# Optimization experiments

Measured on AMD Instinct MI355X. Metric: run time of the kernel, lower is better.

The kernel has to match this reference:

```python
import jax, jax.numpy as jnp
import numpy as np

B, C, HW, A, E, H1, HID = 4096, 4, 64, 32, 4, 1024, 512


def setup_inputs() -> dict:
    key = jax.random.key(0)
    ks = jax.random.split(key, 16)
    def rn(k, shape, fan_in):
        return jax.random.normal(k, shape, dtype=jnp.float32) / np.sqrt(fan_in)
    inp = {
        "x": jax.random.normal(ks[0], (B, C, HW, HW), dtype=jnp.float32),
        # conv stack (OIHW)
        "cW1": rn(ks[1], (32, C, 8, 8), C * 64), "cb1": 0.1 * jnp.ones((32,), jnp.float32),
        "cW2": rn(ks[2], (64, 32, 4, 4), 32 * 16), "cb2": 0.1 * jnp.ones((64,), jnp.float32),
        "cW3": rn(ks[3], (64, 64, 3, 3), 64 * 9), "cb3": 0.1 * jnp.ones((64,), jnp.float32),
        # E expert advantage streams: Linear(1024->512), relu, Linear(512->A)
        "aW1": rn(ks[4], (E, H1, HID), H1), "ab1": jnp.zeros((E, HID), jnp.float32),
        "aW2": rn(ks[5], (E, HID, A), HID), "ab2": jnp.zeros((E, A), jnp.float32),
        # E expert value streams: Linear(1024->512), relu, Linear(512->1)
        "vW1": rn(ks[6], (E, H1, HID), H1), "vb1": jnp.zeros((E, HID), jnp.float32),
        "vW2": rn(ks[7], (E, HID, 1), HID), "vb2": jnp.zeros((E, 1), jnp.float32),
        # reward bucket boundaries (buffer): boundaries * scale - 1e-8
        "boundaries": jnp.array([-0.5, 0.0, 0.5], jnp.float32) * 1.0 - 1e-8,
    }
    return inp


def _conv(h, W, b, stride):
    out = jax.lax.conv_general_dilated(h, W, (stride, stride), "VALID",
                                       dimension_numbers=("NCHW", "OIHW", "NCHW"))
    return out + b[None, :, None, None]


def _routed_mlp(h, W1, b1, W2, b2, idx):
    # h: [B, H1]; W1: [E, H1, HID]; W2: [E, HID, O]; idx: [B]
    # Compute all experts (E is tiny), then gather the routed output per sample.
    z = jax.nn.relu(jnp.einsum("bi,eio->ebo", h, W1) + b1[:, None, :])  # [E,B,HID]
    y = jnp.einsum("ebo,eoa->eba", z, W2) + b2[:, None, :]              # [E,B,O]
    return y[idx, jnp.arange(h.shape[0])]                                # [B,O]


def reference(x, cW1, cb1, cW2, cb2, cW3, cb3, aW1, ab1, aW2, ab2,
              vW1, vb1, vW2, vb2, boundaries):
    h = jax.nn.relu(_conv(x, cW1, cb1, 4))   # [B,32,15,15]
    h = jax.nn.relu(_conv(h, cW2, cb2, 2))   # [B,64,6,6]
    h = jax.nn.relu(_conv(h, cW3, cb3, 1))   # [B,64,4,4]
    bsz = x.shape[0]
    h = h.reshape(bsz, -1)                   # [B,1024]
    rewards = x[:, -1, 0, 0]                 # [B]
    idx = jnp.sum(rewards[:, None] > boundaries[None, :], axis=1)  # [B] in [0,E)
    ya = _routed_mlp(h, aW1, ab1, aW2, ab2, idx)  # [B,A]
    mean = jnp.sum(ya, axis=1, keepdims=True) / ya.shape[1]
    ys = _routed_mlp(h, vW1, vb1, vW2, vb2, idx)  # [B,1]
    q = (ya - mean) + ys
    return q
```

## Files before the change

### kernel.cpp

```cpp
#include <hip/hip_runtime.h>
#include <hip/hip_bf16.h>

typedef __bf16 bf16;
typedef bf16 bf16x8 __attribute__((ext_vector_type(8)));
typedef bf16 bf16x4 __attribute__((ext_vector_type(4)));
typedef float f32x4 __attribute__((ext_vector_type(4)));

__device__ __forceinline__ int SZ(int a) { return a ^ (((a >> 7) & 7) << 4); }

__global__ __launch_bounds__(256) void k_pre(const float* __restrict__ cW1,
    const float* __restrict__ cW2, const float* __restrict__ cW3,
    bf16* __restrict__ W1p, bf16* __restrict__ W2p, bf16* __restrict__ W3p) {
  const int bid = blockIdx.x, tid = threadIdx.x;
  if (bid < 32) {
    int i = bid * 256 + tid;
    int oc = i >> 8, k = i & 255;
    int ic = k & 3, kp = k >> 2, kx = kp & 7, ky = kp >> 3;
    W1p[i] = (bf16)cW1[oc * 256 + ic * 64 + ky * 8 + kx];
  } else if (bid < 160) {
    int i = (bid - 32) * 256 + tid;
    int oc = i >> 9, k = i & 511;
    int ic = k & 31, kp = k >> 5, kx = kp & 3, ky = kp >> 2;
    W2p[i] = (bf16)cW2[oc * 512 + ic * 16 + ky * 4 + kx];
  } else {
    int i = (bid - 160) * 256 + tid;
    if (i < 36864) {
      int oc = i / 576, k = i - oc * 576;
      int ic = k & 63, kp = k >> 6, kx = kp % 3, ky = kp / 3;
      W3p[i] = (bf16)cW3[oc * 576 + ic * 9 + ky * 3 + kx];
    }
  }
}

__global__ __launch_bounds__(256) void k_pre2(const float* __restrict__ aW1,
    const float* __restrict__ vW1, bf16* __restrict__ W1T) {
  __shared__ float t[64][65];
  const int bid2 = blockIdx.x;
  const int bz = bid2 >> 7, rest = bid2 & 127, by = rest >> 4, bx = rest & 15;
  const float* in = (bz >= 4 ? vW1 : aW1) + (size_t)(bz & 3) * 524288;
  const int k0 = bx * 64, n0 = by * 64;
  const int tid = threadIdx.x, cc = tid & 63, r0 = (tid >> 6) * 16;
  for (int i = 0; i < 16; ++i)
    t[r0 + i][cc] = in[(size_t)(k0 + r0 + i) * 512 + n0 + cc];
  __syncthreads();
  for (int i = 0; i < 16; ++i) {
    int n = r0 + i, k = cc;
    W1T[((size_t)bz * 512 + n0 + n) * 1024 + k0 + k] = (bf16)t[k][n];
  }
}

__global__ __launch_bounds__(1024) void k_route(const float* __restrict__ x,
    const float* __restrict__ bd, int* __restrict__ perm, int* __restrict__ cnt) {
  const int tid = threadIdx.x;
  const float t0 = bd[0], t1 = bd[1], t2 = bd[2];
  int e[4];
  #pragma unroll
  for (int i = 0; i < 4; ++i) {
    const int b = tid * 4 + i;
    const float r = x[(size_t)b * 16384 + 12288];
    e[i] = (r > t0) + (r > t1) + (r > t2);
  }
  int lc[4] = {0, 0, 0, 0};
  #pragma unroll
  for (int i = 0; i < 4; ++i) lc[e[i]]++;
  const int lane = tid & 63, wv = tid >> 6;
  __shared__ int wsum[16][4];
  __shared__ int wbase[16][4];
  int pre[4];
  #pragma unroll
  for (int q = 0; q < 4; ++q) {
    int v = lc[q];
    #pragma unroll
    for (int d = 1; d < 64; d <<= 1) {
      int u = __shfl_up(v, d);
      if (lane >= d) v += u;
    }
    pre[q] = v - lc[q];
    if (lane == 63) wsum[wv][q] = v;
  }
  __syncthreads();
  if (tid == 0) {
    int tot[4] = {0, 0, 0, 0};
    for (int w = 0; w < 16; ++w)
      #pragma unroll
      for (int q = 0; q < 4; ++q) { wbase[w][q] = tot[q]; tot[q] += wsum[w][q]; }
    #pragma unroll
    for (int q = 0; q < 4; ++q) cnt[q] = tot[q];
  }
  __syncthreads();
  int run[4];
  #pragma unroll
  for (int q = 0; q < 4; ++q) run[q] = wbase[wv][q] + pre[q];
  #pragma unroll
  for (int i = 0; i < 4; ++i) {
    const int b = tid * 4 + i;
    perm[e[i] * 4096 + run[e[i]]] = b;
    run[e[i]]++;
  }
}

__global__ __launch_bounds__(256, 4) void k_conv1(const float* __restrict__ x,
    const bf16* __restrict__ W1p, const float* __restrict__ b1,
    bf16* __restrict__ h1) {
  __shared__ bf16 sA[16384];
  const int b = blockIdx.x, tid = threadIdx.x;
  const int lane = tid & 63, wave = tid >> 6, lid = lane & 15, c = lane >> 4;
  const int ot = wave & 1, col = ot * 16 + lid;

  bf16x8 bw[8];
  #pragma unroll
  for (int ks = 0; ks < 8; ++ks) bw[ks] = *(const bf16x8*)(W1p + col * 256 + ks * 32 + c * 8);
  const float bias = b1[col];
  #pragma unroll
  for (int ks = 0; ks < 8; ++ks) asm volatile("" : "+v"(bw[ks]));

  {
    const float4* xs = (const float4*)(x + (size_t)b * 16384);
    #pragma unroll
    for (int hb = 0; hb < 2; ++hb) {
      float4 r[2][4];
      #pragma unroll
      for (int h = 0; h < 2; ++h)
        #pragma unroll
        for (int ic = 0; ic < 4; ++ic)
          r[h][ic] = xs[ic * 1024 + tid + (hb * 2 + h) * 256];
      #pragma unroll
      for (int h = 0; h < 2; ++h) {
        const int g = tid + (hb * 2 + h) * 256;
        bf16x8 lo, hi;
        lo[0] = (bf16)r[h][0].x; lo[1] = (bf16)r[h][1].x; lo[2] = (bf16)r[h][2].x; lo[3] = (bf16)r[h][3].x;
        lo[4] = (bf16)r[h][0].y; lo[5] = (bf16)r[h][1].y; lo[6] = (bf16)r[h][2].y; lo[7] = (bf16)r[h][3].y;
        hi[0] = (bf16)r[h][0].z; hi[1] = (bf16)r[h][1].z; hi[2] = (bf16)r[h][2].z; hi[3] = (bf16)r[h][3].z;
        hi[4] = (bf16)r[h][0].w; hi[5] = (bf16)r[h][1].w; hi[6] = (bf16)r[h][2].w; hi[7] = (bf16)r[h][3].w;
        *(bf16x8*)((char*)sA + SZ(g * 32))      = lo;
        *(bf16x8*)((char*)sA + SZ(g * 32 + 16)) = hi;
      }
    }
  }
  __syncthreads();

  int ab[8], ptv[8];
  #pragma unroll
  for (int pi = 0; pi < 8; ++pi) {
    int pt = (wave >> 1) + 2 * pi; if (pt > 14) pt = 14;
    ptv[pi] = pt;
    int p = pt * 16 + lid; if (p > 224) p = 224;
    const int py = p / 15, px = p - py * 15;
    ab[pi] = py * 2048 + px * 32 + c * 16;
  }
  f32x4 acc[8];
  #pragma unroll
  for (int pi = 0; pi < 8; ++pi) acc[pi] = (f32x4){0.f, 0.f, 0.f, 0.f};
  #pragma unroll
  for (int ks = 0; ks < 8; ++ks)
    #pragma unroll
    for (int pi = 0; pi < 8; ++pi)
      acc[pi] = __builtin_amdgcn_mfma_f32_16x16x32_bf16(
          *(const bf16x8*)((const char*)sA + SZ(ab[pi] + ks * 512)), bw[ks], acc[pi], 0, 0, 0);
  __syncthreads();

  #pragma unroll
  for (int pi = 0; pi < 8; ++pi)
    #pragma unroll
    for (int r = 0; r < 4; ++r) {
      const int pr = ptv[pi] * 16 + c * 4 + r;
      if (pr < 225) sA[pr * 32 + col] = (bf16)fmaxf(acc[pi][r] + bias, 0.f);
    }
  __syncthreads();

  bf16* hb = h1 + (size_t)b * 7200;
  for (int i = tid; i < 900; i += 256)
    *(bf16x8*)(hb + i * 8) = *(const bf16x8*)(&sA[i * 8]);
}

__global__ __launch_bounds__(256, 3) void k_conv23(const bf16* __restrict__ h1,
    const bf16* __restrict__ W2p, const float* __restrict__ b2,
    const bf16* __restrict__ W3p, const float* __restrict__ b3,
    bf16* __restrict__ h3) {
  __shared__ bf16 sh1[2][9000];
  __shared__ bf16 sh2[2][2592];
  const int b0 = blockIdx.x * 2, tid = threadIdx.x;
  const int lane = tid & 63, wave = tid >> 6, lid = lane & 15, c = lane >> 4;
  const int col = wave * 16 + lid;

  bf16x8 bw2[16];
  #pragma unroll
  for (int ks = 0; ks < 16; ++ks) bw2[ks] = *(const bf16x8*)(W2p + col * 512 + ks * 32 + c * 8);
  const float bias2 = b2[col];
  #pragma unroll
  for (int ks = 0; ks < 16; ++ks) asm volatile("" : "+v"(bw2[ks]));

  for (int i = tid; i < 1800; i += 256) {
    const int img = (i >= 900), j = i - img * 900;
    const int pix = j >> 2, part = j & 3;
    *(bf16x8*)(&sh1[img][pix * 40 + part * 8]) =
        *(const bf16x8*)(h1 + (size_t)(b0 + img) * 7200 + j * 8);
  }
  __syncthreads();

  f32x4 acc2[2][3];
  #pragma unroll
  for (int g = 0; g < 2; ++g)
    #pragma unroll
    for (int pt = 0; pt < 3; ++pt) acc2[g][pt] = (f32x4){0.f, 0.f, 0.f, 0.f};
  #pragma unroll
  for (int g = 0; g < 2; ++g) {
    int abase[3];
    #pragma unroll
    for (int pt = 0; pt < 3; ++pt) {
      int p = pt * 16 + lid; if (p > 35) p = 35;
      const int oy = p / 6, ox = p - oy * 6;
      abase[pt] = (oy * 30 + ox * 2) * 40 + c * 8;
    }
    #pragma unroll
    for (int ks = 0; ks < 16; ++ks) {
      const int ky = ks >> 2, kx = ks & 3;
      #pragma unroll
      for (int pt = 0; pt < 3; ++pt)
        acc2[g][pt] = __builtin_amdgcn_mfma_f32_16x16x32_bf16(
            *(const bf16x8*)(&sh1[g][abase[pt] + (ky * 15 + kx) * 40]), bw2[ks],
            acc2[g][pt], 0, 0, 0);
    }
  }
  #pragma unroll
  for (int g = 0; g < 2; ++g)
    #pragma unroll
    for (int pt = 0; pt < 3; ++pt)
      #pragma unroll
      for (int r = 0; r < 4; ++r) {
        const int pr = pt * 16 + c * 4 + r;
        if (pr < 36) sh2[g][pr * 72 + col] = (bf16)fmaxf(acc2[g][pt][r] + bias2, 0.f);
      }
  __syncthreads();

  bf16x8 bw3[18];
  #pragma unroll
  for (int ks = 0; ks < 18; ++ks) bw3[ks] = *(const bf16x8*)(W3p + col * 576 + ks * 32 + c * 8);
  const float bias3 = b3[col];
  const int oy = lid >> 2, ox = lid & 3;
  const int ab3 = (oy * 6 + ox) * 72 + c * 8;
  #pragma unroll
  for (int g = 0; g < 2; ++g) {
    f32x4 acc = {0.f, 0.f, 0.f, 0.f};
    #pragma unroll
    for (int ks = 0; ks < 18; ++ks) {
      const int kp = ks >> 1, ky = kp / 3, kx = kp - ky * 3;
      acc = __builtin_amdgcn_mfma_f32_16x16x32_bf16(
          *(const bf16x8*)(&sh2[g][ab3 + (ky * 6 + kx) * 72 + (ks & 1) * 32]), bw3[ks],
          acc, 0, 0, 0);
    }
    bf16x4 o;
    #pragma unroll
    for (int r = 0; r < 4; ++r) o[r] = (bf16)fmaxf(acc[r] + bias3, 0.f);
    *(bf16x4*)(h3 + (size_t)(b0 + g) * 1024 + col * 16 + c * 4) = o;
  }
}

__global__ __launch_bounds__(512) void k_mlp1(const bf16* __restrict__ h3,
    const bf16* __restrict__ W1T, const float* __restrict__ ab1, const float* __restrict__ vb1,
    const int* __restrict__ perm, const int* __restrict__ cnt,
    bf16* __restrict__ za, bf16* __restrict__ zv) {
  const int e = blockIdx.z;
  const int cntE = cnt[e];
  const int m0 = blockIdx.x * 64;
  if (m0 >= cntE) return;
  const int n0 = blockIdx.y * 128;
  const bf16* WA = W1T + (size_t)e * 524288;
  const bf16* WV = W1T + (size_t)(4 + e) * 524288;

  __shared__ bf16 As[64 * 72];
  __shared__ int rows[64];
  const int tid = threadIdx.x;
  if (tid < 64) {
    int j = m0 + tid; if (j > cntE - 1) j = cntE - 1;
    rows[tid] = perm[e * 4096 + j];
  }
  __syncthreads();

  const int lane = tid & 63, wave = tid >> 6;
  const int lid = lane & 15, c = lane >> 4;
  const int wm = wave >> 2, wn = wave & 3;
  const int srow = tid >> 3, skoff = (tid & 7) * 8;
  const bf16* arow = h3 + (size_t)rows[srow] * 1024 + skoff;
  const int colA = n0 + wn * 32 + lid;
  const bf16* wa0 = WA + (size_t)colA * 1024 + c * 8;
  const bf16* wa1 = WA + (size_t)(colA + 16) * 1024 + c * 8;
  const bf16* wv0 = WV + (size_t)colA * 1024 + c * 8;
  const bf16* wv1 = WV + (size_t)(colA + 16) * 1024 + c * 8;
  const int ar0 = (wm * 32 + lid) * 72 + c * 8;
  const int ar1 = (wm * 32 + 16 + lid) * 72 + c * 8;

  f32x4 acc[2][2][2];
  #pragma unroll
  for (int n = 0; n < 2; ++n)
    #pragma unroll
    for (int m = 0; m < 2; ++m)
      #pragma unroll
      for (int f = 0; f < 2; ++f) acc[n][m][f] = (f32x4){0.f, 0.f, 0.f, 0.f};

  for (int k0 = 0; k0 < 1024; k0 += 64) {
    *(bf16x8*)(&As[srow * 72 + skoff]) = *(const bf16x8*)(arow + k0);
    __syncthreads();
    bf16x8 a[2][2];
    #pragma unroll
    for (int m = 0; m < 2; ++m)
      #pragma unroll
      for (int ks = 0; ks < 2; ++ks)
        a[m][ks] = *(const bf16x8*)(&As[(m ? ar1 : ar0) + ks * 32]);
    #pragma unroll
    for (int ks = 0; ks < 2; ++ks) {
      bf16x8 bA0 = *(const bf16x8*)(wa0 + k0 + ks * 32);
      bf16x8 bA1 = *(const bf16x8*)(wa1 + k0 + ks * 32);
      bf16x8 bV0 = *(const bf16x8*)(wv0 + k0 + ks * 32);
      bf16x8 bV1 = *(const bf16x8*)(wv1 + k0 + ks * 32);
      #pragma unroll
      for (int m = 0; m < 2; ++m) {
        acc[0][m][0] = __builtin_amdgcn_mfma_f32_16x16x32_bf16(a[m][ks], bA0, acc[0][m][0], 0, 0, 0);
        acc[0][m][1] = __builtin_amdgcn_mfma_f32_16x16x32_bf16(a[m][ks], bA1, acc[0][m][1], 0, 0, 0);
        acc[1][m][0] = __builtin_amdgcn_mfma_f32_16x16x32_bf16(a[m][ks], bV0, acc[1][m][0], 0, 0, 0);
        acc[1][m][1] = __builtin_amdgcn_mfma_f32_16x16x32_bf16(a[m][ks], bV1, acc[1][m][1], 0, 0, 0);
      }
    }
    __syncthreads();
  }

  #pragma unroll
  for (int cf = 0; cf < 2; ++cf) {
    const int col = colA + cf * 16;
    const float bA = ab1[e * 512 + col];
    const float bV = vb1[e * 512 + col];
    #pragma unroll
    for (int m = 0; m < 2; ++m)
      #pragma unroll
      for (int r = 0; r < 4; ++r) {
        const int ridx = wm * 32 + m * 16 + c * 4 + r;
        if (m0 + ridx < cntE) {
          const size_t zoff = (size_t)rows[ridx] * 512 + col;
          za[zoff] = (bf16)fmaxf(acc[0][m][cf][r] + bA, 0.f);
          zv[zoff] = (bf16)fmaxf(acc[1][m][cf][r] + bV, 0.f);
        }
      }
  }
}

__global__ __launch_bounds__(256) void k_mlp2(const bf16* __restrict__ za,
    const bf16* __restrict__ zv,
    const float* __restrict__ aW2, const float* __restrict__ ab2,
    const float* __restrict__ vW2, const float* __restrict__ vb2,
    const int* __restrict__ perm, const int* __restrict__ cnt,
    float* __restrict__ out) {
  const int e = blockIdx.y;
  const int cntE = cnt[e];
  const int m0 = blockIdx.x * 64;
  if (m0 >= cntE) return;
  __shared__ bf16 Bs[48 * 520];
  const int tid = threadIdx.x;
  for (int i = tid; i < 512 * 32; i += 256) {
    const int k = i >> 5, n = i & 31;
    Bs[n * 520 + k] = (bf16)aW2[(size_t)e * 16384 + i];
  }
  for (int i = tid; i < 512; i += 256) Bs[32 * 520 + i] = (bf16)vW2[e * 512 + i];
  for (int i = tid; i < 15 * 512; i += 256) {
    const int n = 33 + (i >> 9), k = i & 511;
    Bs[n * 520 + k] = (bf16)0.f;
  }
  __syncthreads();

  const int lane = tid & 63, wave = tid >> 6;
  const int lid = lane & 15, c = lane >> 4;
  const int row0 = m0 + wave * 16;
  if (row0 >= cntE) return;
  int rowl = row0 + lid; if (rowl > cntE - 1) rowl = cntE - 1;
  const int pb = perm[e * 4096 + rowl];
  const bf16* aA = za + (size_t)pb * 512 + c * 8;
  const bf16* aV = zv + (size_t)pb * 512 + c * 8;

  f32x4 acc0 = {0.f, 0.f, 0.f, 0.f}, acc1 = acc0, accv = acc0;
  #pragma unroll
  for (int k0 = 0; k0 < 512; k0 += 32) {
    bf16x8 a1 = *(const bf16x8*)(aA + k0);
    bf16x8 a2 = *(const bf16x8*)(aV + k0);
    bf16x8 b0 = *(const bf16x8*)(&Bs[lid * 520 + k0 + c * 8]);
    bf16x8 b1 = *(const bf16x8*)(&Bs[(16 + lid) * 520 + k0 + c * 8]);
    bf16x8 b2 = *(const bf16x8*)(&Bs[(32 + lid) * 520 + k0 + c * 8]);
    acc0 = __builtin_amdgcn_mfma_f32_16x16x32_bf16(a1, b0, acc0, 0, 0, 0);
    acc1 = __builtin_amdgcn_mfma_f32_16x16x32_bf16(a1, b1, acc1, 0, 0, 0);
    accv = __builtin_amdgcn_mfma_f32_16x16x32_bf16(a2, b2, accv, 0, 0, 0);
  }

  const float ba0 = ab2[e * 32 + lid], ba1 = ab2[e * 32 + 16 + lid], bv = vb2[e];
  #pragma unroll
  for (int r = 0; r < 4; ++r) {
    const int row = row0 + c * 4 + r;
    const float y0 = acc0[r] + ba0, y1 = acc1[r] + ba1;
    float s = y0 + y1;
    s += __shfl_xor(s, 1); s += __shfl_xor(s, 2);
    s += __shfl_xor(s, 4); s += __shfl_xor(s, 8);
    const float mean = s * 0.03125f;
    const float ys = __shfl(accv[r], lane & 48) + bv;
    if (row < cntE) {
      const int bq = perm[e * 4096 + row];
      out[(size_t)bq * 32 + lid] = y0 - mean + ys;
      out[(size_t)bq * 32 + 16 + lid] = y1 - mean + ys;
    }
  }
}

extern "C" void kernel_launch(void* const* d_in, const int* in_sizes, int n_in,
                              void* d_out, int out_size, void* d_ws, size_t ws_size,
                              hipStream_t stream) {
  const float* x   = (const float*)d_in[0];
  const float* cW1 = (const float*)d_in[1];
  const float* cb1 = (const float*)d_in[2];
  const float* cW2 = (const float*)d_in[3];
  const float* cb2 = (const float*)d_in[4];
  const float* cW3 = (const float*)d_in[5];
  const float* cb3 = (const float*)d_in[6];
  const float* aW1 = (const float*)d_in[7];
  const float* ab1 = (const float*)d_in[8];
  const float* aW2 = (const float*)d_in[9];
  const float* ab2 = (const float*)d_in[10];
  const float* vW1 = (const float*)d_in[11];
  const float* vb1 = (const float*)d_in[12];
  const float* vW2 = (const float*)d_in[13];
  const float* vb2 = (const float*)d_in[14];
  const float* bd  = (const float*)d_in[15];
  float* out = (float*)d_out;

  char* ws = (char*)d_ws;
  bf16* h1  = (bf16*)(ws);
  bf16* W1T = (bf16*)(ws);
  bf16* za  = (bf16*)(ws + 8388608ull);
  bf16* zv  = (bf16*)(ws + 12582912ull);
  bf16* h3  = (bf16*)(ws + 58982400ull);
  bf16* W1p = (bf16*)(ws + 67371008ull);
  bf16* W2p = (bf16*)(ws + 67387392ull);
  bf16* W3p = (bf16*)(ws + 67452928ull);
  int* perm = (int*)(ws + 67526656ull);
  int* cnt  = (int*)(ws + 67592192ull);

  k_pre<<<304, 256, 0, stream>>>(cW1, cW2, cW3, W1p, W2p, W3p);
  k_route<<<1, 1024, 0, stream>>>(x, bd, perm, cnt);
  k_conv1<<<4096, 256, 0, stream>>>(x, W1p, cb1, h1);
  k_conv23<<<2048, 256, 0, stream>>>(h1, W2p, cb2, W3p, cb3, h3);
  k_pre2<<<1024, 256, 0, stream>>>(aW1, vW1, W1T);
  k_mlp1<<<dim3(64, 4, 4), 512, 0, stream>>>(h3, W1T, ab1, vb1, perm, cnt, za, zv);
  k_mlp2<<<dim3(64, 4), 256, 0, stream>>>(za, zv, aW2, ab2, vW2, vb2, perm, cnt, out);
}
```

Baseline: 211.1 us.

## Fuse conv1, conv2 and conv3 into one kernel keeping activations in LDS

Merges the conv1 kernel and the two-image conv2/conv3 kernel into one per-image kernel. The conv1 output stays in shared memory and is never written to global memory and read back, which removes about 59 MB of h1 round-trip traffic and one launch. LDS per block grows to about 50 KB and occupancy drops from 4 to 3 blocks. Each block now does one image of conv2/3 instead of two, so weight registers are reloaded per image. The workspace is compacted, and k_pre2 is moved earlier because W1T no longer aliases h1.

```diff
diff --git a/kernel.cpp b/kernel.cpp
--- a/kernel.cpp
+++ b/kernel.cpp
@@ -99,22 +99,25 @@
   }
 }
 
-__global__ __launch_bounds__(256, 4) void k_conv1(const float* __restrict__ x,
+__global__ __launch_bounds__(256, 3) void k_conv123(const float* __restrict__ x,
     const bf16* __restrict__ W1p, const float* __restrict__ b1,
-    bf16* __restrict__ h1) {
+    const bf16* __restrict__ W2p, const float* __restrict__ b2,
+    const bf16* __restrict__ W3p, const float* __restrict__ b3,
+    bf16* __restrict__ h3) {
   __shared__ bf16 sA[16384];
+  __shared__ bf16 sh1[9000];
   const int b = blockIdx.x, tid = threadIdx.x;
   const int lane = tid & 63, wave = tid >> 6, lid = lane & 15, c = lane >> 4;
-  const int ot = wave & 1, col = ot * 16 + lid;
-
-  bf16x8 bw[8];
-  #pragma unroll
-  for (int ks = 0; ks < 8; ++ks) bw[ks] = *(const bf16x8*)(W1p + col * 256 + ks * 32 + c * 8);
-  const float bias = b1[col];
-  #pragma unroll
-  for (int ks = 0; ks < 8; ++ks) asm volatile("" : "+v"(bw[ks]));
 
   {
+    bf16x8 bw[8];
+    const int ot = wave & 1, col = ot * 16 + lid;
+    #pragma unroll
+    for (int ks = 0; ks < 8; ++ks) bw[ks] = *(const bf16x8*)(W1p + col * 256 + ks * 32 + c * 8);
+    const float bias = b1[col];
+    #pragma unroll
+    for (int ks = 0; ks < 8; ++ks) asm volatile("" : "+v"(bw[ks]));
+
     const float4* xs = (const float4*)(x + (size_t)b * 16384);
     #pragma unroll
     for (int hb = 0; hb < 2; ++hb) {
@@ -136,75 +139,47 @@
         *(bf16x8*)((char*)sA + SZ(g * 32 + 16)) = hi;
       }
     }
-  }
-  __syncthreads();
-
-  int ab[8], ptv[8];
-  #pragma unroll
-  for (int pi = 0; pi < 8; ++pi) {
-    int pt = (wave >> 1) + 2 * pi; if (pt > 14) pt = 14;
-    ptv[pi] = pt;
-    int p = pt * 16 + lid; if (p > 224) p = 224;
-    const int py = p / 15, px = p - py * 15;
-    ab[pi] = py * 2048 + px * 32 + c * 16;
-  }
-  f32x4 acc[8];
-  #pragma unroll
-  for (int pi = 0; pi < 8; ++pi) acc[pi] = (f32x4){0.f, 0.f, 0.f, 0.f};
-  #pragma unroll
-  for (int ks = 0; ks < 8; ++ks)
+    __syncthreads();
+
+    int ab[8], ptv[8];
+    #pragma unroll
+    for (int pi = 0; pi < 8; ++pi) {
+      int pt = (wave >> 1) + 2 * pi; if (pt > 14) pt = 14;
+      ptv[pi] = pt;
+      int p = pt * 16 + lid; if (p > 224) p = 224;
+      const int py = p / 15, px = p - py * 15;
+      ab[pi] = py * 2048 + px * 32 + c * 16;
+    }
+    f32x4 acc[8];
+    #pragma unroll
+    for (int pi = 0; pi < 8; ++pi) acc[pi] = (f32x4){0.f, 0.f, 0.f, 0.f};
+    #pragma unroll
+    for (int ks = 0; ks < 8; ++ks)
+      #pragma unroll
+      for (int pi = 0; pi < 8; ++pi)
+        acc[pi] = __builtin_amdgcn_mfma_f32_16x16x32_bf16(
+            *(const bf16x8*)((const char*)sA + SZ(ab[pi] + ks * 512)), bw[ks], acc[pi], 0, 0, 0);
+    __syncthreads();
     #pragma unroll
     for (int pi = 0; pi < 8; ++pi)
-      acc[pi] = __builtin_amdgcn_mfma_f32_16x16x32_bf16(
-          *(const bf16x8*)((const char*)sA + SZ(ab[pi] + ks * 512)), bw[ks], acc[pi], 0, 0, 0);
-  __syncthreads();
-
-  #pragma unroll
-  for (int pi = 0; pi < 8; ++pi)
-    #pragma unroll
-    for (int r = 0; r < 4; ++r) {
-      const int pr = ptv[pi] * 16 + c * 4 + r;
-      if (pr < 225) sA[pr * 32 + col] = (bf16)fmaxf(acc[pi][r] + bias, 0.f);
-    }
-  __syncthreads();
-
-  bf16* hb = h1 + (size_t)b * 7200;
-  for (int i = tid; i < 900; i += 256)
-    *(bf16x8*)(hb + i * 8) = *(const bf16x8*)(&sA[i * 8]);
-}
-
-__global__ __launch_bounds__(256, 3) void k_conv23(const bf16* __restrict__ h1,
-    const bf16* __restrict__ W2p, const float* __restrict__ b2,
-    const bf16* __restrict__ W3p, const float* __restrict__ b3,
-    bf16* __restrict__ h3) {
-  __shared__ bf16 sh1[2][9000];
-  __shared__ bf16 sh2[2][2592];
-  const int b0 = blockIdx.x * 2, tid = threadIdx.x;
-  const int lane = tid & 63, wave = tid >> 6, lid = lane & 15, c = lane >> 4;
+      #pragma unroll
+      for (int r = 0; r < 4; ++r) {
+        const int pr = ptv[pi] * 16 + c * 4 + r;
+        if (pr < 225) sh1[pr * 40 + col] = (bf16)fmaxf(acc[pi][r] + bias, 0.f);
+      }
+  }
+  __syncthreads();
+
+  bf16* sh2 = sA;
   const int col = wave * 16 + lid;
-
-  bf16x8 bw2[16];
-  #pragma unroll
-  for (int ks = 0; ks < 16; ++ks) bw2[ks] = *(const bf16x8*)(W2p + col * 512 + ks * 32 + c * 8);
-  const float bias2 = b2[col];
-  #pragma unroll
-  for (int ks = 0; ks < 16; ++ks) asm volatile("" : "+v"(bw2[ks]));
-
-  for (int i = tid; i < 1800; i += 256) {
-    const int img = (i >= 900), j = i - img * 900;
-    const int pix = j >> 2, part = j & 3;
-    *(bf16x8*)(&sh1[img][pix * 40 + part * 8]) =
-        *(const bf16x8*)(h1 + (size_t)(b0 + img) * 7200 + j * 8);
-  }
-  __syncthreads();
-
-  f32x4 acc2[2][3];
-  #pragma unroll
-  for (int g = 0; g < 2; ++g)
-    #pragma unroll
-    for (int pt = 0; pt < 3; ++pt) acc2[g][pt] = (f32x4){0.f, 0.f, 0.f, 0.f};
-  #pragma unroll
-  for (int g = 0; g < 2; ++g) {
+  {
+    bf16x8 bw2[16];
+    #pragma unroll
+    for (int ks = 0; ks < 16; ++ks) bw2[ks] = *(const bf16x8*)(W2p + col * 512 + ks * 32 + c * 8);
+    const float bias2 = b2[col];
+    #pragma unroll
+    for (int ks = 0; ks < 16; ++ks) asm volatile("" : "+v"(bw2[ks]));
+
     int abase[3];
     #pragma unroll
     for (int pt = 0; pt < 3; ++pt) {
@@ -212,47 +187,47 @@
       const int oy = p / 6, ox = p - oy * 6;
       abase[pt] = (oy * 30 + ox * 2) * 40 + c * 8;
     }
+    f32x4 acc2[3];
+    #pragma unroll
+    for (int pt = 0; pt < 3; ++pt) acc2[pt] = (f32x4){0.f, 0.f, 0.f, 0.f};
     #pragma unroll
     for (int ks = 0; ks < 16; ++ks) {
       const int ky = ks >> 2, kx = ks & 3;
       #pragma unroll
       for (int pt = 0; pt < 3; ++pt)
-        acc2[g][pt] = __builtin_amdgcn_mfma_f32_16x16x32_bf16(
-            *(const bf16x8*)(&sh1[g][abase[pt] + (ky * 15 + kx) * 40]), bw2[ks],
-            acc2[g][pt], 0, 0, 0);
-    }
-  }
-  #pragma unroll
-  for (int g = 0; g < 2; ++g)
+        acc2[pt] = __builtin_amdgcn_mfma_f32_16x16x32_bf16(
+            *(const bf16x8*)(&sh1[abase[pt] + (ky * 15 + kx) * 40]), bw2[ks], acc2[pt], 0, 0, 0);
+    }
     #pragma unroll
     for (int pt = 0; pt < 3; ++pt)
       #pragma unroll
       for (int r = 0; r < 4; ++r) {
         const int pr = pt * 16 + c * 4 + r;
-        if (pr < 36) sh2[g][pr * 72 + col] = (bf16)fmaxf(acc2[g][pt][r] + bias2, 0.f);
+        if (pr < 36) sh2[pr * 72 + col] = (bf16)fmaxf(acc2[pt][r] + bias2, 0.f);
       }
-  __syncthreads();
-
-  bf16x8 bw3[18];
-  #pragma unroll
-  for (int ks = 0; ks < 18; ++ks) bw3[ks] = *(const bf16x8*)(W3p + col * 576 + ks * 32 + c * 8);
-  const float bias3 = b3[col];
-  const int oy = lid >> 2, ox = lid & 3;
-  const int ab3 = (oy * 6 + ox) * 72 + c * 8;
-  #pragma unroll
-  for (int g = 0; g < 2; ++g) {
+  }
+  __syncthreads();
+
+  {
+    bf16x8 bw3[18];
+    #pragma unroll
+    for (int ks = 0; ks < 18; ++ks) bw3[ks] = *(const bf16x8*)(W3p + col * 576 + ks * 32 + c * 8);
+    const float bias3 = b3[col];
+    #pragma unroll
+    for (int ks = 0; ks < 18; ++ks) asm volatile("" : "+v"(bw3[ks]));
+    const int oy = lid >> 2, ox = lid & 3;
+    const int ab3 = (oy * 6 + ox) * 72 + c * 8;
     f32x4 acc = {0.f, 0.f, 0.f, 0.f};
     #pragma unroll
     for (int ks = 0; ks < 18; ++ks) {
       const int kp = ks >> 1, ky = kp / 3, kx = kp - ky * 3;
       acc = __builtin_amdgcn_mfma_f32_16x16x32_bf16(
-          *(const bf16x8*)(&sh2[g][ab3 + (ky * 6 + kx) * 72 + (ks & 1) * 32]), bw3[ks],
-          acc, 0, 0, 0);
+          *(const bf16x8*)(&sh2[ab3 + (ky * 6 + kx) * 72 + (ks & 1) * 32]), bw3[ks], acc, 0, 0, 0);
     }
     bf16x4 o;
     #pragma unroll
     for (int r = 0; r < 4; ++r) o[r] = (bf16)fmaxf(acc[r] + bias3, 0.f);
-    *(bf16x4*)(h3 + (size_t)(b0 + g) * 1024 + col * 16 + c * 4) = o;
+    *(bf16x4*)(h3 + (size_t)b * 1024 + col * 16 + c * 4) = o;
   }
 }
 
@@ -428,22 +403,20 @@
   float* out = (float*)d_out;
 
   char* ws = (char*)d_ws;
-  bf16* h1  = (bf16*)(ws);
   bf16* W1T = (bf16*)(ws);
   bf16* za  = (bf16*)(ws + 8388608ull);
   bf16* zv  = (bf16*)(ws + 12582912ull);
-  bf16* h3  = (bf16*)(ws + 58982400ull);
-  bf16* W1p = (bf16*)(ws + 67371008ull);
-  bf16* W2p = (bf16*)(ws + 67387392ull);
-  bf16* W3p = (bf16*)(ws + 67452928ull);
-  int* perm = (int*)(ws + 67526656ull);
-  int* cnt  = (int*)(ws + 67592192ull);
+  bf16* h3  = (bf16*)(ws + 16777216ull);
+  bf16* W1p = (bf16*)(ws + 25165824ull);
+  bf16* W2p = (bf16*)(ws + 25182208ull);
+  bf16* W3p = (bf16*)(ws + 25247744ull);
+  int* perm = (int*)(ws + 25321472ull);
+  int* cnt  = (int*)(ws + 25387008ull);
 
   k_pre<<<304, 256, 0, stream>>>(cW1, cW2, cW3, W1p, W2p, W3p);
+  k_pre2<<<1024, 256, 0, stream>>>(aW1, vW1, W1T);
   k_route<<<1, 1024, 0, stream>>>(x, bd, perm, cnt);
-  k_conv1<<<4096, 256, 0, stream>>>(x, W1p, cb1, h1);
-  k_conv23<<<2048, 256, 0, stream>>>(h1, W2p, cb2, W3p, cb3, h3);
-  k_pre2<<<1024, 256, 0, stream>>>(aW1, vW1, W1T);
+  k_conv123<<<4096, 256, 0, stream>>>(x, W1p, cb1, W2p, cb2, W3p, cb3, h3);
   k_mlp1<<<dim3(64, 4, 4), 512, 0, stream>>>(h3, W1T, ab1, vb1, perm, cnt, za, zv);
   k_mlp2<<<dim3(64, 4), 256, 0, stream>>>(za, zv, aW2, ab2, vW2, vb2, perm, cnt, out);
 }
```

Result: no change. 207.4 us (-1.7%).
